# Optimization experiments

Measured on AMD Instinct MI355X. Metric: run time of the kernel, lower is better.

## Reference

```python
import jax, jax.numpy as jnp
from jax import lax
import numpy as np

B, T_IN, T_OUT = 16, 16, 16
C, H, W = 3, 64, 64
ZDIM, HID = 128, 512
DN = ('NCHW', 'OIHW', 'NCHW')


def setup_inputs() -> dict:
    key = jax.random.key(0)
    ks = iter(jax.random.split(key, 64))
    rn = lambda shape, s: jax.random.normal(next(ks), shape, jnp.float32) * s
    cs, ls = 0.05, 0.04  # conv / lstm weight scales
    inp = {
        'video': jax.random.uniform(next(ks), (B, T_IN, C, H, W), jnp.float32),
        'target_len': T_OUT,
        'ec1_w': rn((32, 3, 4, 4), cs),   'ec1_b': jnp.zeros((32,)),
        'ec2_w': rn((64, 32, 4, 4), cs),  'ec2_b': jnp.zeros((64,)),
        'ec3_w': rn((128, 64, 4, 4), cs), 'ec3_b': jnp.zeros((128,)),
        'ec4_w': rn((256, 128, 4, 4), cs),'ec4_b': jnp.zeros((256,)),
        'fcmu_w': rn((ZDIM, 4096), 0.02), 'fcmu_b': jnp.zeros((ZDIM,)),
        'dfc_w': rn((4096, ZDIM), 0.02),  'dfc_b': jnp.zeros((4096,)),
        'dt1_w': rn((128, 256, 4, 4), cs),'dt1_b': jnp.zeros((128,)),
        'dt2_w': rn((64, 128, 4, 4), cs), 'dt2_b': jnp.zeros((64,)),
        'dt3_w': rn((32, 64, 4, 4), cs),  'dt3_b': jnp.zeros((32,)),
        'dt4_w': rn((3, 32, 4, 4), cs),   'dt4_b': jnp.zeros((3,)),
        'wih_e': rn((4 * HID, ZDIM), ls), 'whh_e': rn((4 * HID, HID), ls),
        'bih_e': jnp.zeros((4 * HID,)),   'bhh_e': jnp.zeros((4 * HID,)),
        'wih_d': rn((4 * HID, ZDIM), ls), 'whh_d': rn((4 * HID, HID), ls),
        'bih_d': jnp.zeros((4 * HID,)),   'bhh_d': jnp.zeros((4 * HID,)),
        'fc_w': rn((ZDIM, HID), ls),      'fc_b': jnp.zeros((ZDIM,)),
    }
    return inp


def _conv(x, w, b):
    y = lax.conv_general_dilated(x, w, (2, 2), ((1, 1), (1, 1)), dimension_numbers=DN)
    return y + b[None, :, None, None]


def _convt(x, w, b):
    # transposed conv (stride 2, k=4, p=1) as input-dilated conv: out = 2*in
    y = lax.conv_general_dilated(x, w, (1, 1), ((2, 2), (2, 2)),
                                 lhs_dilation=(2, 2), dimension_numbers=DN)
    return y + b[None, :, None, None]


def _lstm_cell(x, h, c, wih, whh, bih, bhh):
    g = x @ wih.T + h @ whh.T + bih + bhh  # [N, 4H]
    i, f, gg, o = jnp.split(g, 4, axis=-1)  # torch gate order i,f,g,o
    c = jax.nn.sigmoid(f) * c + jax.nn.sigmoid(i) * jnp.tanh(gg)
    h = jax.nn.sigmoid(o) * jnp.tanh(c)
    return h, c


def reference(video, target_len,
              ec1_w, ec1_b, ec2_w, ec2_b, ec3_w, ec3_b, ec4_w, ec4_b,
              fcmu_w, fcmu_b, dfc_w, dfc_b,
              dt1_w, dt1_b, dt2_w, dt2_b, dt3_w, dt3_b, dt4_w, dt4_b,
              wih_e, whh_e, bih_e, bhh_e, wih_d, whh_d, bih_d, bhh_d,
              fc_w, fc_b):
    b, t = video.shape[:2]

    def encode(frames):  # [N, 3, 64, 64] -> [N, ZDIM] (z = mu, deterministic)
        x = jax.nn.relu(_conv(frames, ec1_w, ec1_b))
        x = jax.nn.relu(_conv(x, ec2_w, ec2_b))
        x = jax.nn.relu(_conv(x, ec3_w, ec3_b))
        x = jax.nn.relu(_conv(x, ec4_w, ec4_b))  # [N, 256, 4, 4]
        x = x.reshape(x.shape[0], -1)
        return x @ fcmu_w.T + fcmu_b

    def decode(z):  # [N, ZDIM] -> [N, 3, 64, 64]
        x = jax.nn.relu(z @ dfc_w.T + dfc_b).reshape(-1, 256, 4, 4)
        x = jax.nn.relu(_convt(x, dt1_w, dt1_b))
        x = jax.nn.relu(_convt(x, dt2_w, dt2_b))
        x = jax.nn.relu(_convt(x, dt3_w, dt3_b))
        return jax.nn.sigmoid(_convt(x, dt4_w, dt4_b))

    z = encode(video.reshape(b * t, C, H, W)).reshape(b, t, ZDIM)

    # encoder LSTM over input sequence
    def enc_step(carry, x_t):
        h, c = carry
        h, c = _lstm_cell(x_t, h, c, wih_e, whh_e, bih_e, bhh_e)
        return (h, c), None
    h0 = jnp.zeros((b, HID), video.dtype)
    (h, c), _ = lax.scan(enc_step, (h0, h0), z.transpose(1, 0, 2))

    def dec_step(carry, _):
        hh, cc, x = carry
        hh, cc = _lstm_cell(x, hh, cc, wih_d, whh_d, bih_d, bhh_d)
        out = hh @ fc_w.T + fc_b
        return (hh, cc, out), out
    _, zs = lax.scan(dec_step, (h, c, z[:, -1]), None, length=target_len)
    zs = zs.transpose(1, 0, 2).reshape(b * target_len, ZDIM)

    predicted = decode(zs).reshape(b, target_len, C, H, W)
    return predicted
```

## Files before the change

kernel.cpp:

```cpp
#include <hip/hip_runtime.h>
#include <math.h>


typedef float f32x4 __attribute__((ext_vector_type(4)));
typedef short bf16x8 __attribute__((ext_vector_type(8)));

__device__ __forceinline__ float sig_(float x) { return 1.f / (1.f + expf(-x)); }
__device__ __forceinline__ float dot4(float4 a, float4 b) {
    return a.x * b.x + a.y * b.y + a.z * b.z + a.w * b.w;
}
__device__ __forceinline__ int orig_row(int c) {
    return ((c >> 2) & 3) * 512 + (c >> 4) * 4 + (c & 3);
}
__device__ __forceinline__ unsigned short f2bf(float f) {
    unsigned int b = __float_as_uint(f);
    return (unsigned short)((b + 0x7fffu + ((b >> 16) & 1u)) >> 16);
}
__device__ __forceinline__ float bf2f(unsigned short h) {
    return __uint_as_float(((unsigned int)h) << 16);
}
__device__ __forceinline__ float4 bf4_to_f4(uint2 u) {
    float4 r;
    r.x = __uint_as_float((u.x & 0xffffu) << 16);
    r.y = __uint_as_float(u.x & 0xffff0000u);
    r.z = __uint_as_float((u.y & 0xffffu) << 16);
    r.w = __uint_as_float(u.y & 0xffff0000u);
    return r;
}

template<int CIP, int HI, int WI, int CO, int MREP, int WM, int WN, int MODE, int SRCF32>
__global__ __launch_bounds__(64 * WM * WN)
void conv_mfma(const unsigned short* __restrict__ Ahi, const float* __restrict__ Af,
               const unsigned short* __restrict__ WB, const float* __restrict__ bias,
               unsigned short* __restrict__ Yhi) {
    constexpr int K    = CIP * (MODE ? 4 : 16);
    constexpr int K32  = K / 32;
    constexpr int NI   = 2 * MREP;
    constexpr int TAPS = MODE ? 4 : 16;
    constexpr int CC   = (CIP >= 32) ? CIP / 32 : 1;
    constexpr int HO   = MODE ? HI * 2 : HI / 2;
    constexpr int WO   = MODE ? WI * 2 : WI / 2;
    constexpr int SH   = MODE ? HI : HI / 2;
    constexpr int SW   = MODE ? WI : WI / 2;
    constexpr int HWS  = SH * SW;
    constexpr int MT   = (256 * HWS) / (32 * MREP * WM);
    constexpr int NT   = CO / (32 * WN);
    constexpr int PLANE = CO * K;

    int bid = blockIdx.x;
    int mt = bid % MT; bid /= MT;
    int nt = bid % NT; int par = bid / NT;
    int p = par >> 1, q = par & 1;

    int tid = threadIdx.x;
    int lane = tid & 63, wid = tid >> 6;
    int wm = wid % WM, wn = wid / WM;
    int mbase = mt * (32 * MREP * WM) + wm * (32 * MREP);
    int nbase = nt * (32 * WN) + wn * 32;
    int lm = lane & 15, lg = lane >> 4;

    int ani[NI], asy[NI], asx[NI];
#pragma unroll
    for (int i = 0; i < NI; ++i) {
        int m = mbase + 16 * i + lm;
        ani[i] = m / HWS; int r = m % HWS; asy[i] = r / SW; asx[i] = r % SW;
    }

    f32x4 acc[NI][2];
#pragma unroll
    for (int i = 0; i < NI; ++i)
#pragma unroll
        for (int j = 0; j < 2; ++j)
#pragma unroll
            for (int e = 0; e < 4; ++e) acc[i][j][e] = 0.f;

    const unsigned short* WBp = WB + (long)par * 2 * PLANE;

    if constexpr (SRCF32) {
        for (int kb = 0; kb < K; kb += 32) {
            int k0 = kb + lg * 8;
            int t0 = k0 >> 2;
            bf16x8 ah[NI];
#pragma unroll
            for (int i = 0; i < NI; ++i) {
                float f[8];
#pragma unroll
                for (int h = 0; h < 2; ++h) {
                    int tap = t0 + h;
                    int ih = 2 * asy[i] + (tap >> 2) - 1;
                    int iw = 2 * asx[i] + (tap & 3) - 1;
                    float4 v = {0.f, 0.f, 0.f, 0.f};
                    if ((unsigned)ih < (unsigned)HI && (unsigned)iw < (unsigned)WI)
                        v = *(const float4*)(Af + (((long)ani[i] * HI + ih) * WI + iw) * 4);
                    f[h * 4 + 0] = v.x; f[h * 4 + 1] = v.y;
                    f[h * 4 + 2] = v.z; f[h * 4 + 3] = v.w;
                }
#pragma unroll
                for (int e = 0; e < 8; ++e) ah[i][e] = (short)f2bf(f[e]);
            }
            bf16x8 bh[2], bl[2];
#pragma unroll
            for (int j = 0; j < 2; ++j) {
                long bidx = ((long)((nbase >> 4) + j) * K32 + (kb >> 5)) * 512 + lane * 8;
                bh[j] = *(const bf16x8*)(WBp + bidx);
                bl[j] = *(const bf16x8*)(WBp + PLANE + bidx);
            }
#pragma unroll
            for (int i = 0; i < NI; ++i)
#pragma unroll
                for (int j = 0; j < 2; ++j) {
                    acc[i][j] = __builtin_amdgcn_mfma_f32_16x16x32_bf16(ah[i], bh[j], acc[i][j], 0, 0, 0);
                    acc[i][j] = __builtin_amdgcn_mfma_f32_16x16x32_bf16(ah[i], bl[j], acc[i][j], 0, 0, 0);
                }
        }
    } else {
        long abase[NI]; unsigned vmask[NI];
#pragma unroll
        for (int i = 0; i < NI; ++i) {
            abase[i] = (long)ani[i] * HI * WI * CIP;
            unsigned vm = 0;
#pragma unroll
            for (int t = 0; t < TAPS; ++t) {
                int iy, ix;
                if constexpr (MODE == 0) {
                    iy = 2 * asy[i] + (t >> 2) - 1; ix = 2 * asx[i] + (t & 3) - 1;
                } else {
                    iy = asy[i] + p + (t >> 1) - 1; ix = asx[i] + q + (t & 1) - 1;
                }
                if (iy >= 0 && iy < HI && ix >= 0 && ix < WI) vm |= (1u << t);
            }
            vmask[i] = vm;
        }
#pragma unroll 2
        for (int tap = 0; tap < TAPS; ++tap) {
            int dy, dx;
            if constexpr (MODE == 0) { dy = (tap >> 2) - 1; dx = (tap & 3) - 1; }
            else { dy = p + (tap >> 1) - 1; dx = q + (tap & 1) - 1; }
            long roff[NI]; unsigned msk[NI];
#pragma unroll
            for (int i = 0; i < NI; ++i) {
                int iy = (MODE == 0 ? 2 * asy[i] : asy[i]) + dy;
                int ix = (MODE == 0 ? 2 * asx[i] : asx[i]) + dx;
                int iyc = min(max(iy, 0), HI - 1);
                int ixc = min(max(ix, 0), WI - 1);
                roff[i] = abase[i] + ((long)iyc * WI + ixc) * CIP + lg * 8;
                msk[i] = ((vmask[i] >> tap) & 1u) ? 0xffffffffu : 0u;
            }
#pragma unroll
            for (int cc = 0; cc < CC; ++cc) {
                int kb32 = tap * CC + cc;
                bf16x8 ah[NI];
#pragma unroll
                for (int i = 0; i < NI; ++i) {
                    uint4 u = *(const uint4*)(Ahi + roff[i] + cc * 32);
                    u.x &= msk[i]; u.y &= msk[i]; u.z &= msk[i]; u.w &= msk[i];
                    ah[i] = *(bf16x8*)&u;
                }
                bf16x8 bh[2], bl[2];
#pragma unroll
                for (int j = 0; j < 2; ++j) {
                    long bidx = ((long)((nbase >> 4) + j) * K32 + kb32) * 512 + lane * 8;
                    bh[j] = *(const bf16x8*)(WBp + bidx);
                    bl[j] = *(const bf16x8*)(WBp + PLANE + bidx);
                }
#pragma unroll
                for (int i = 0; i < NI; ++i)
#pragma unroll
                    for (int j = 0; j < 2; ++j) {
                        acc[i][j] = __builtin_amdgcn_mfma_f32_16x16x32_bf16(ah[i], bh[j], acc[i][j], 0, 0, 0);
                        acc[i][j] = __builtin_amdgcn_mfma_f32_16x16x32_bf16(ah[i], bl[j], acc[i][j], 0, 0, 0);
                    }
            }
        }
    }

#pragma unroll
    for (int i = 0; i < NI; ++i)
#pragma unroll
        for (int j = 0; j < 2; ++j)
#pragma unroll
            for (int r = 0; r < 4; ++r) {
                int m = mbase + 16 * i + lg * 4 + r;
                int co = nbase + 16 * j + lm;
                float v = fmaxf(acc[i][j][r] + bias[co], 0.f);
                long off;
                if constexpr (MODE == 0) {
                    off = (long)m * CO + co;
                } else {
                    int ni = m / HWS; int rm = m % HWS;
                    int oy = 2 * (rm / SW) + p, ox = 2 * (rm % SW) + q;
                    off = (((long)ni * HO + oy) * WO + ox) * CO + co;
                }
                Yhi[off] = f2bf(v);
            }
}

__global__ __launch_bounds__(128)
void dt4_tiled(const unsigned short* __restrict__ Xh,
               const float4* __restrict__ Wd, const float* __restrict__ bias,
               float* __restrict__ out) {
    __shared__ uint2 xt[8 * 205];
    int bid = blockIdx.x;
    int n = bid >> 3, yg = bid & 7;
    int y0 = yg * 4;
    int tid = threadIdx.x;
    long nb = (long)n * 32768;
    for (int j = tid; j < 1632; j += 128) {
        int c4 = j & 7; int pos = j >> 3;
        int r = pos / 34, cc = pos % 34;
        int ih = y0 - 1 + r, iw = cc - 1;
        uint2 u = {0u, 0u};
        if ((unsigned)ih < 32u && (unsigned)iw < 32u)
            u = *(const uint2*)(Xh + nb + ((long)ih * 32 + iw) * 32 + c4 * 4);
        xt[c4 * 205 + pos] = u;
    }
    __syncthreads();
    int ly = tid >> 5, lx = tid & 31;
    float acc[3][4];
#pragma unroll
    for (int j = 0; j < 3; ++j) {
        float b = bias[j];
#pragma unroll
        for (int par = 0; par < 4; ++par) acc[j][par] = b;
    }
#pragma unroll
    for (int ci4 = 0; ci4 < 8; ++ci4) {
        float4 xv[9];
        int base = ci4 * 205 + ly * 34 + lx;
#pragma unroll
        for (int r = 0; r < 3; ++r)
#pragma unroll
            for (int c = 0; c < 3; ++c)
                xv[r * 3 + c] = bf4_to_f4(xt[base + r * 34 + c]);
        const float4* wp = Wd + ci4 * 48;
#pragma unroll
        for (int j = 0; j < 3; ++j)
#pragma unroll
            for (int par = 0; par < 4; ++par) {
                int p = par >> 1, q = par & 1;
#pragma unroll
                for (int t4 = 0; t4 < 4; ++t4) {
                    int dh = t4 >> 1, dw = t4 & 1;
                    acc[j][par] += dot4(xv[(p + dh) * 3 + (q + dw)],
                                        wp[(j * 4 + par) * 4 + t4]);
                }
            }
    }
    int yy = y0 + ly, xx = lx;
#pragma unroll
    for (int j = 0; j < 3; ++j)
#pragma unroll
        for (int p = 0; p < 2; ++p) {
            float2 v;
            v.x = sig_(acc[j][p * 2 + 0]);
            v.y = sig_(acc[j][p * 2 + 1]);
            *(float2*)(out + (((long)n * 3 + j) * 64 + 2 * yy + p) * 64 + 2 * xx) = v;
        }
}

__global__ void prep_packs(const float* __restrict__ ec3_w, const float* __restrict__ ec4_w,
                           const float* __restrict__ dt1_w, const float* __restrict__ dt2_w,
                           unsigned short* __restrict__ WBe3, unsigned short* __restrict__ WBe4,
                           unsigned short* __restrict__ WBd1, unsigned short* __restrict__ WBd2) {
    int idx = blockIdx.x * 256 + threadIdx.x;
    if (idx < 131072) {
        int li = idx;
        int j = li & 7, lane = (li >> 3) & 63;
        int kb = (li >> 9) & 31, nt = li >> 14;
        int k = kb * 32 + (lane >> 4) * 8 + j;
        int tap = k >> 6, ci = k & 63;
        int co = nt * 16 + (lane & 15);
        float f = ec3_w[((long)co * 64 + ci) * 16 + tap];
        unsigned short hi = f2bf(f);
        WBe3[li] = hi; WBe3[131072 + li] = f2bf(f - bf2f(hi));
    } else if (idx < 655360) {
        int li = idx - 131072;
        int j = li & 7, lane = (li >> 3) & 63;
        int kb = (li >> 9) & 63, nt = li >> 15;
        int k = kb * 32 + (lane >> 4) * 8 + j;
        int tap = k >> 7, ci = k & 127;
        int co = nt * 16 + (lane & 15);
        float f = ec4_w[((long)co * 128 + ci) * 16 + tap];
        unsigned short hi = f2bf(f);
        WBe4[li] = hi; WBe4[524288 + li] = f2bf(f - bf2f(hi));
    } else if (idx < 1179648) {
        int li = idx - 655360;
        int par = li >> 17; int rem = li & 131071;
        int j = rem & 7, lane = (rem >> 3) & 63;
        int kb = (rem >> 9) & 31, nt = rem >> 14;
        int k = kb * 32 + (lane >> 4) * 8 + j;
        int t4 = k >> 8, ci = k & 255;
        int p = par >> 1, q = par & 1, dh = t4 >> 1, dw = t4 & 1;
        int tap = (p + 2 * dh) * 4 + (q + 2 * dw);
        int co = nt * 16 + (lane & 15);
        float f = dt1_w[((long)co * 256 + ci) * 16 + tap];
        unsigned short hi = f2bf(f);
        WBd1[(long)par * 262144 + rem] = hi;
        WBd1[(long)par * 262144 + 131072 + rem] = f2bf(f - bf2f(hi));
    } else if (idx < 1310720) {
        int li = idx - 1179648;
        int par = li >> 15; int rem = li & 32767;
        int j = rem & 7, lane = (rem >> 3) & 63;
        int kb = (rem >> 9) & 15, nt = rem >> 13;
        int k = kb * 32 + (lane >> 4) * 8 + j;
        int t4 = k >> 7, ci = k & 127;
        int p = par >> 1, q = par & 1, dh = t4 >> 1, dw = t4 & 1;
        int tap = (p + 2 * dh) * 4 + (q + 2 * dw);
        int co = nt * 16 + (lane & 15);
        float f = dt2_w[((long)co * 128 + ci) * 16 + tap];
        unsigned short hi = f2bf(f);
        WBd2[(long)par * 65536 + rem] = hi;
        WBd2[(long)par * 65536 + 32768 + rem] = f2bf(f - bf2f(hi));
    }
}

__global__ void prep_tail(const float* __restrict__ ec1_w, const float* __restrict__ ec2_w,
                          const float* __restrict__ dt3_w, const float* __restrict__ dt4_w,
                          unsigned short* __restrict__ WBe1, unsigned short* __restrict__ WBe2,
                          unsigned short* __restrict__ WBd3, float4* __restrict__ WTd4) {
    int idx = blockIdx.x * 256 + threadIdx.x;
    if (idx < 2048) {
        int li = idx;
        int j = li & 7, lane = (li >> 3) & 63;
        int kb = (li >> 9) & 1, nt = li / 1024;
        int k = kb * 32 + (lane >> 4) * 8 + j;
        int tap = k >> 2, ci = k & 3;
        int co = nt * 16 + (lane & 15);
        float f = (ci < 3) ? ec1_w[((long)co * 3 + ci) * 16 + tap] : 0.f;
        unsigned short hi = f2bf(f);
        WBe1[li] = hi; WBe1[2048 + li] = f2bf(f - bf2f(hi));
    } else if (idx < 34816) {
        int li = idx - 2048;
        int j = li & 7, lane = (li >> 3) & 63;
        int kb = (li >> 9) & 15, nt = li / 8192;
        int k = kb * 32 + (lane >> 4) * 8 + j;
        int tap = k >> 5, ci = k & 31;
        int co = nt * 16 + (lane & 15);
        float f = ec2_w[((long)co * 32 + ci) * 16 + tap];
        unsigned short hi = f2bf(f);
        WBe2[li] = hi; WBe2[32768 + li] = f2bf(f - bf2f(hi));
    } else if (idx < 67584) {
        int li = idx - 34816;
        int par = li >> 13; int rem = li & 8191;
        int j = rem & 7, lane = (rem >> 3) & 63;
        int kb = (rem >> 9) & 7, nt = rem >> 12;
        int k = kb * 32 + (lane >> 4) * 8 + j;
        int t4 = k >> 6, ci = k & 63;
        int p = par >> 1, q = par & 1, dh = t4 >> 1, dw = t4 & 1;
        int tap = (p + 2 * dh) * 4 + (q + 2 * dw);
        int co = nt * 16 + (lane & 15);
        float f = dt3_w[((long)co * 64 + ci) * 16 + tap];
        unsigned short hi = f2bf(f);
        WBd3[par * 16384 + rem] = hi;
        WBd3[par * 16384 + 8192 + rem] = f2bf(f - bf2f(hi));
    } else if (idx < 67968) {
        int li = idx - 67584;
        int t4 = li & 3, par = (li >> 2) & 3;
        int co = (li >> 4) % 3, ci4 = (li >> 4) / 3;
        int p = par >> 1, q = par & 1, dh = t4 >> 1, dw = t4 & 1;
        int tap = (p + 2 * dh) * 4 + (q + 2 * dw);
        float4 v; float* pv = (float*)&v;
#pragma unroll
        for (int l = 0; l < 4; ++l)
            pv[l] = dt4_w[((long)co * 32 + ci4 * 4 + l) * 16 + tap];
        WTd4[li] = v;
    }
}

__global__ void prep_r1(const float* __restrict__ wih_e, const float* __restrict__ wih_d,
                        const float* __restrict__ fc_w,
                        const float* __restrict__ bih_d, const float* __restrict__ bhh_d,
                        const float* __restrict__ fc_b,
                        const float* __restrict__ fcmu_w, const float* __restrict__ dfc_w,
                        const float* __restrict__ dfc_b,
                        float* __restrict__ WIHP_E, float* __restrict__ WIHP_D,
                        float* __restrict__ FCP, float* __restrict__ BIASDC,
                        float* __restrict__ FCMUP, float* __restrict__ DFCP,
                        float* __restrict__ DFCB) {
    int idx = blockIdx.x * 256 + threadIdx.x;
    if (idx < 262144) {
        int c = idx & 2047, m = idx >> 11;
        WIHP_E[idx] = wih_e[orig_row(c) * 128 + m];
    } else if (idx < 524288) {
        int li = idx - 262144;
        int c = li & 2047, m = li >> 11;
        WIHP_D[li] = wih_d[orig_row(c) * 128 + m];
    } else if (idx < 589824) {
        int li = idx - 524288;
        int r = li & 127, c = li >> 7;
        FCP[li] = fc_w[(long)r * 512 + c];
    } else if (idx < 591872) {
        int c = idx - 589824;
        int orow = orig_row(c);
        float s = bih_d[orow] + bhh_d[orow];
        for (int m = 0; m < 128; ++m) s += fc_b[m] * wih_d[orow * 128 + m];
        BIASDC[c] = s;
    } else if (idx < 1116160) {
        int li = idx - 591872;
        int j = li & 127, k = li >> 7;
        FCMUP[li] = fcmu_w[(long)j * 4096 + (k & 255) * 16 + (k >> 8)];
    } else {
        int li = idx - 1116160;
        int j = li & 4095, m = li >> 12;
        int jc = (j & 255) * 16 + (j >> 8);
        DFCP[li] = dfc_w[(long)jc * 128 + m];
        if (li < 4096) DFCB[li] = dfc_b[(li & 255) * 16 + (li >> 8)];
    }
}

__global__ void to_nhwc4v(const float* __restrict__ v, float4* __restrict__ out) {
    int idx = blockIdx.x * 256 + threadIdx.x;
    int w = idx & 63, h = (idx >> 6) & 63, n = idx >> 12;
    long base = (long)n * 12288 + h * 64 + w;
    float4 o;
    o.x = v[base];
    o.y = v[base + 4096];
    o.z = v[base + 8192];
    o.w = 0.f;
    out[idx] = o;
}

__global__ void pack_whh(const float* __restrict__ whh, float4* __restrict__ out) {
    int idx = blockIdx.x * 256 + threadIdx.x;
    int c = idx & 2047, k4 = idx >> 11;
    const float4* src = (const float4*)(whh + orig_row(c) * 512);
    out[idx] = src[k4];
}

__global__ __launch_bounds__(256)
void merge_dc(const float* __restrict__ wih_d, const float* __restrict__ fc_w,
              const float* __restrict__ whh_d, float* __restrict__ out) {
    int cb = (blockIdx.x >> 3) * 64, kb = (blockIdx.x & 7) * 64;
    int tid = threadIdx.x;
    int cgl = (tid & 15) * 4, kgl = (tid >> 4) * 4;
    __shared__ float At[64][65];
    __shared__ float Bt[64][65];
    float acc[4][4] = {};
    for (int mc = 0; mc < 128; mc += 64) {
        __syncthreads();
        for (int i = tid; i < 4096; i += 256) {
            int cl = i >> 6, m = i & 63;
            At[cl][m] = wih_d[orig_row(cb + cl) * 128 + mc + m];
            Bt[cl][m] = fc_w[(mc + cl) * 512 + kb + m];
        }
        __syncthreads();
        for (int m = 0; m < 64; ++m) {
            float a[4], b[4];
#pragma unroll
            for (int i = 0; i < 4; ++i) { a[i] = At[cgl + i][m]; b[i] = Bt[m][kgl + i]; }
#pragma unroll
            for (int i = 0; i < 4; ++i)
#pragma unroll
                for (int j = 0; j < 4; ++j) acc[i][j] += a[i] * b[j];
        }
    }
    for (int i = 0; i < 4; ++i) {
        int c = cb + cgl + i; int orow = orig_row(c);
        for (int j = 0; j < 4; ++j) {
            int k = kb + kgl + j;
            out[((k >> 2) * 2048 + c) * 4 + (k & 3)] = acc[i][j] + whh_d[orow * 512 + k];
        }
    }
}

__global__ __launch_bounds__(512)
void gx2_kernel(const float* __restrict__ Z,
                const float* __restrict__ wE, const float* __restrict__ biE,
                const float* __restrict__ bhE,
                const float* __restrict__ wD, const float* __restrict__ biD,
                const float* __restrict__ bhD,
                float* __restrict__ gxe, float* __restrict__ gxd0) {
    __shared__ float zl[2048];
    int bid = blockIdx.x, tid = threadIdx.x;
    if (bid < 128) {
        int rg = bid >> 2, cch = bid & 3;
        for (int i = tid; i < 1024; i += 512)
            zl[i] = Z[(long)(rg * 8 + (i >> 7)) * 128 + (i & 127)];
        __syncthreads();
        int c = cch * 512 + tid;
        int orow = orig_row(c);
        float bsum = biE[orow] + bhE[orow];
        float acc[8];
#pragma unroll
        for (int r = 0; r < 8; ++r) acc[r] = bsum;
        for (int m = 0; m < 128; ++m) {
            float wv = wE[m * 2048 + c];
#pragma unroll
            for (int r = 0; r < 8; ++r) acc[r] += zl[r * 128 + m] * wv;
        }
        for (int r = 0; r < 8; ++r) gxe[(long)(rg * 8 + r) * 2048 + c] = acc[r];
    } else {
        int cch = bid - 128;
        for (int i = tid; i < 2048; i += 512)
            zl[i] = Z[(long)((i >> 7) * 16 + 15) * 128 + (i & 127)];
        __syncthreads();
        int c = cch * 512 + tid;
        int orow = orig_row(c);
        float bsum = biD[orow] + bhD[orow];
        float acc[16];
#pragma unroll
        for (int r = 0; r < 16; ++r) acc[r] = bsum;
        for (int m = 0; m < 128; ++m) {
            float wv = wD[m * 2048 + c];
#pragma unroll
            for (int r = 0; r < 16; ++r) acc[r] += zl[r * 128 + m] * wv;
        }
        for (int r = 0; r < 16; ++r) gxd0[(long)r * 2048 + c] = acc[r];
    }
}

__global__ __launch_bounds__(256)
void lstm_step(const float4* __restrict__ wh4, const float* __restrict__ gadd,
               int gstride, const float* __restrict__ h_in, float* __restrict__ h_out,
               float* __restrict__ cst, float* __restrict__ hall) {
    __shared__ float hs[8192];
    __shared__ float gb[16][16];
    int tid = threadIdx.x;
    float4* hs4 = (float4*)hs;
    const float4* hi4 = (const float4*)h_in;
#pragma unroll
    for (int i = 0; i < 8; ++i) hs4[tid + 256 * i] = hi4[tid + 256 * i];
    __syncthreads();
    int col = tid & 15, n = tid >> 4;
    int cg = blockIdx.x * 16 + col;
    float acc = gadd[n * gstride + cg];
    const float4* wp = wh4 + cg;
    const float4* hv = (const float4*)(hs + n * 512);
#pragma unroll 8
    for (int k4 = 0; k4 < 128; ++k4) {
        float4 wv = wp[(long)k4 * 2048];
        float4 h4 = hv[k4];
        acc += wv.x * h4.x + wv.y * h4.y + wv.z * h4.z + wv.w * h4.w;
    }
    gb[n][col] = acc;
    __syncthreads();
    if (col < 4) {
        int j = blockIdx.x * 4 + col;
        float gi = sig_(gb[n][col]);
        float gf = sig_(gb[n][col + 4]);
        float gg = tanhf(gb[n][col + 8]);
        float go = sig_(gb[n][col + 12]);
        int idx = n * 512 + j;
        float cv = gf * cst[idx] + gi * gg;
        cst[idx] = cv;
        float hvv = go * tanhf(cv);
        h_out[idx] = hvv;
        if (hall) hall[idx] = hvv;
    }
}

__global__ __launch_bounds__(512)
void fcmu_part(const unsigned short* __restrict__ xh,
               const float* __restrict__ wP, float* __restrict__ part) {
    int rg = blockIdx.x >> 4, ks = blockIdx.x & 15;
    int tid = threadIdx.x;
    __shared__ float xls[16 * 256];
    for (int i = tid; i < 4096; i += 512) {
        long gi = (long)(rg * 16 + (i >> 8)) * 4096 + ks * 256 + (i & 255);
        xls[i] = bf2f(xh[gi]);
    }
    __syncthreads();
    int j = tid & 127, rq = tid >> 7;
    float acc[4] = {0, 0, 0, 0};
    for (int k = 0; k < 256; ++k) {
        float wv = wP[(ks * 256 + k) * 128 + j];
#pragma unroll
        for (int i = 0; i < 4; ++i) acc[i] += xls[(rq + 4 * i) * 256 + k] * wv;
    }
    for (int i = 0; i < 4; ++i)
        part[((long)ks * 256 + rg * 16 + rq + 4 * i) * 128 + j] = acc[i];
}

__global__ void fcmu_red(const float* __restrict__ part, const float* __restrict__ b,
                         float* __restrict__ z) {
    int idx = blockIdx.x * 256 + threadIdx.x;
    float s = b[idx & 127];
    for (int k = 0; k < 16; ++k) s += part[k * 32768 + idx];
    z[idx] = s;
}

__global__ __launch_bounds__(512)
void zs_k(const float* __restrict__ hall, const float* __restrict__ fcP,
          const float* __restrict__ fcb, float* __restrict__ zs) {
    int t = blockIdx.x >> 2, nq = blockIdx.x & 3;
    int tid = threadIdx.x;
    __shared__ float hs[4 * 512];
    const float* h = hall + (long)t * 8192 + nq * 2048;
    for (int i = tid; i < 2048; i += 512) hs[i] = h[i];
    __syncthreads();
    int j = tid & 127, nl = tid >> 7;
    float a0 = 0.f, a1 = 0.f, a2 = 0.f, a3 = 0.f;
    const float* hr = hs + nl * 512;
    for (int k = 0; k < 512; k += 4) {
        a0 += hr[k] * fcP[k * 128 + j];
        a1 += hr[k + 1] * fcP[(k + 1) * 128 + j];
        a2 += hr[k + 2] * fcP[(k + 2) * 128 + j];
        a3 += hr[k + 3] * fcP[(k + 3) * 128 + j];
    }
    int n = nq * 4 + nl;
    zs[((long)n * 16 + t) * 128 + j] = (a0 + a1) + (a2 + a3) + fcb[j];
}

__global__ __launch_bounds__(256)
void dfc_k(const float* __restrict__ zs, const float* __restrict__ dP,
           const float* __restrict__ db, unsigned short* __restrict__ outh) {
    int rg = blockIdx.x >> 4, jc = blockIdx.x & 15;
    int tid = threadIdx.x;
    __shared__ float zl[512];
    for (int i = tid; i < 512; i += 256) zl[i] = zs[(long)rg * 512 + i];
    __syncthreads();
    int j = jc * 256 + tid;
    float acc[4] = {0.f, 0.f, 0.f, 0.f};
    for (int m = 0; m < 128; ++m) {
        float wv = dP[(long)m * 4096 + j];
#pragma unroll
        for (int r = 0; r < 4; ++r) acc[r] += zl[r * 128 + m] * wv;
    }
    float bv = db[j];
    for (int r = 0; r < 4; ++r) {
        float v = fmaxf(acc[r] + bv, 0.f);
        outh[(long)(rg * 4 + r) * 4096 + j] = f2bf(v);
    }
}

extern "C" void kernel_launch(void* const* d_in, const int* in_sizes, int n_in,
                              void* d_out, int out_size, void* d_ws, size_t ws_size,
                              hipStream_t stream) {
    (void)in_sizes; (void)n_in; (void)out_size; (void)ws_size;
    const float* video  = (const float*)d_in[0];
    const float* ec1_w  = (const float*)d_in[2];  const float* ec1_b = (const float*)d_in[3];
    const float* ec2_w  = (const float*)d_in[4];  const float* ec2_b = (const float*)d_in[5];
    const float* ec3_w  = (const float*)d_in[6];  const float* ec3_b = (const float*)d_in[7];
    const float* ec4_w  = (const float*)d_in[8];  const float* ec4_b = (const float*)d_in[9];
    const float* fcmu_w = (const float*)d_in[10]; const float* fcmu_b = (const float*)d_in[11];
    const float* dfc_w  = (const float*)d_in[12]; const float* dfc_b = (const float*)d_in[13];
    const float* dt1_w  = (const float*)d_in[14]; const float* dt1_b = (const float*)d_in[15];
    const float* dt2_w  = (const float*)d_in[16]; const float* dt2_b = (const float*)d_in[17];
    const float* dt3_w  = (const float*)d_in[18]; const float* dt3_b = (const float*)d_in[19];
    const float* dt4_w  = (const float*)d_in[20]; const float* dt4_b = (const float*)d_in[21];
    const float* wih_e  = (const float*)d_in[22]; const float* whh_e = (const float*)d_in[23];
    const float* bih_e  = (const float*)d_in[24]; const float* bhh_e = (const float*)d_in[25];
    const float* wih_d  = (const float*)d_in[26]; const float* whh_d = (const float*)d_in[27];
    const float* bih_d  = (const float*)d_in[28]; const float* bhh_d = (const float*)d_in[29];
    const float* fc_w   = (const float*)d_in[30]; const float* fc_b  = (const float*)d_in[31];

    char* wsb = (char*)d_ws;
    unsigned short* B1h = (unsigned short*)wsb;
    float*          X0f = (float*)(wsb + 33554432);
    unsigned short* B2h = (unsigned short*)(wsb + 33554432);
    unsigned short* B3h = (unsigned short*)(wsb + 50331648);
    unsigned short* B4h = (unsigned short*)(wsb + 58720256);
    float* R1f    = (float*)wsb;
    float* WH4_E  = R1f;
    float* WH4_DC = R1f + 1048576;
    float* WIHP_E = R1f + 2097152;
    float* WIHP_D = R1f + 2359296;
    float* GX_E   = R1f + 2621440;
    float* GX_D0  = R1f + 3145728;
    float* BIASDC = R1f + 3178496;
    float* HA     = R1f + 3180544;
    float* HB     = R1f + 3188736;
    float* CB     = R1f + 3196928;
    float* HALL   = R1f + 3205120;
    float* FCMUP  = R1f + 3336192;
    float* FCP    = R1f + 4122624;
    float* DFCP   = R1f + 4188160;
    float* DFCB   = R1f + 4712448;
    float* Z      = R1f + 4716544;
    float* ZS     = R1f + 4749312;
    unsigned short* WBe3 = (unsigned short*)(R1f + 4782080);
    unsigned short* WBe4 = (unsigned short*)(R1f + 4913152);
    unsigned short* WBd1 = (unsigned short*)(R1f + 5437440);
    unsigned short* WBd2 = (unsigned short*)(R1f + 5961728);
    float* ZPART  = R1f + 6092800;
    unsigned short* WBe1 = (unsigned short*)(wsb + 62914560);
    unsigned short* WBe2 = (unsigned short*)(wsb + 62922752);
    unsigned short* WBd3 = (unsigned short*)(wsb + 63053824);
    float*          WTd4 = (float*)(wsb + 63184896);

    prep_tail<<<266, 256, 0, stream>>>(ec1_w, ec2_w, dt3_w, dt4_w,
                                       WBe1, WBe2, WBd3, (float4*)WTd4);
    to_nhwc4v<<<4096, 256, 0, stream>>>(video, (float4*)X0f);
    conv_mfma<4, 64, 64, 32, 2, 4, 1, 0, 1><<<1024, 256, 0, stream>>>(
        nullptr, X0f, WBe1, ec1_b, B1h);
    conv_mfma<32, 32, 32, 64, 1, 2, 2, 0, 0><<<1024, 256, 0, stream>>>(
        B1h, nullptr, WBe2, ec2_b, B2h);

    prep_r1<<<6408, 256, 0, stream>>>(wih_e, wih_d, fc_w, bih_d, bhh_d, fc_b,
                                      fcmu_w, dfc_w, dfc_b,
                                      WIHP_E, WIHP_D, FCP, BIASDC, FCMUP, DFCP, DFCB);
    prep_packs<<<5120, 256, 0, stream>>>(ec3_w, ec4_w, dt1_w, dt2_w,
                                         WBe3, WBe4, WBd1, WBd2);
    pack_whh<<<1024, 256, 0, stream>>>(whh_e, (float4*)WH4_E);
    merge_dc<<<256, 256, 0, stream>>>(wih_d, fc_w, whh_d, WH4_DC);
    hipMemsetAsync(HA, 0, 3 * 8192 * sizeof(float), stream);

    conv_mfma<64, 16, 16, 128, 1, 2, 2, 0, 0><<<512, 256, 0, stream>>>(
        B2h, nullptr, WBe3, ec3_b, B3h);
    conv_mfma<128, 8, 8, 256, 1, 1, 2, 0, 0><<<512, 128, 0, stream>>>(
        B3h, nullptr, WBe4, ec4_b, B4h);
    fcmu_part<<<256, 512, 0, stream>>>(B4h, FCMUP, ZPART);
    fcmu_red<<<128, 256, 0, stream>>>(ZPART, fcmu_b, Z);

    gx2_kernel<<<132, 512, 0, stream>>>(Z, WIHP_E, bih_e, bhh_e,
                                        WIHP_D, bih_d, bhh_d, GX_E, GX_D0);

    float* hin = HA; float* hout = HB;
    for (int t = 0; t < 16; ++t) {
        lstm_step<<<128, 256, 0, stream>>>((const float4*)WH4_E, GX_E + t * 2048, 32768,
                                           hin, hout, CB, (float*)nullptr);
        float* tmp = hin; hin = hout; hout = tmp;
    }
    pack_whh<<<1024, 256, 0, stream>>>(whh_d, (float4*)WH4_E);
    lstm_step<<<128, 256, 0, stream>>>((const float4*)WH4_E, GX_D0, 2048,
                                       hin, hout, CB, HALL);
    { float* tmp = hin; hin = hout; hout = tmp; }
    for (int t = 1; t < 16; ++t) {
        lstm_step<<<128, 256, 0, stream>>>((const float4*)WH4_DC, BIASDC, 0,
                                           hin, hout, CB, HALL + t * 8192);
        float* tmp = hin; hin = hout; hout = tmp;
    }
    zs_k<<<64, 512, 0, stream>>>(HALL, FCP, fc_b, ZS);

    dfc_k<<<1024, 256, 0, stream>>>(ZS, DFCP, DFCB, B4h);
    conv_mfma<256, 4, 4, 128, 1, 2, 2, 1, 0><<<512, 256, 0, stream>>>(
        B4h, nullptr, WBd1, dt1_b, B3h);
    conv_mfma<128, 8, 8, 64, 1, 2, 2, 1, 0><<<1024, 256, 0, stream>>>(
        B3h, nullptr, WBd2, dt2_b, B2h);
    conv_mfma<64, 16, 16, 32, 2, 4, 1, 1, 0><<<1024, 256, 0, stream>>>(
        B2h, nullptr, WBd3, dt3_b, B1h);
    dt4_tiled<<<2048, 128, 0, stream>>>(B1h, (const float4*)WTd4, dt4_b, (float*)d_out);
}
```

Measured before the change: 601.5 us.

## Split LSTM step across twice the blocks with K-split and regrouped gate columns

After: 535.8 us. 10.9% less time.

```diff
diff --git a/kernel.cpp b/kernel.cpp
--- a/kernel.cpp
+++ b/kernel.cpp
@@ -10,7 +10,7 @@
     return a.x * b.x + a.y * b.y + a.z * b.z + a.w * b.w;
 }
 __device__ __forceinline__ int orig_row(int c) {
-    return ((c >> 2) & 3) * 512 + (c >> 4) * 4 + (c & 3);
+    return ((c >> 1) & 3) * 512 + (c >> 3) * 2 + (c & 1);
 }
 __device__ __forceinline__ unsigned short f2bf(float f) {
     unsigned int b = __float_as_uint(f);
@@ -514,33 +514,41 @@
                int gstride, const float* __restrict__ h_in, float* __restrict__ h_out,
                float* __restrict__ cst, float* __restrict__ hall) {
     __shared__ float hs[8192];
-    __shared__ float gb[16][16];
+    __shared__ float gp[2][16][8];
     int tid = threadIdx.x;
     float4* hs4 = (float4*)hs;
     const float4* hi4 = (const float4*)h_in;
 #pragma unroll
     for (int i = 0; i < 8; ++i) hs4[tid + 256 * i] = hi4[tid + 256 * i];
     __syncthreads();
-    int col = tid & 15, n = tid >> 4;
-    int cg = blockIdx.x * 16 + col;
-    float acc = gadd[n * gstride + cg];
+    int col = tid & 7, n = (tid >> 3) & 15, kh = tid >> 7;
+    int cg = blockIdx.x * 8 + col;
     const float4* wp = wh4 + cg;
     const float4* hv = (const float4*)(hs + n * 512);
+    float acc = 0.f;
+    int k0 = kh * 64;
 #pragma unroll 8
-    for (int k4 = 0; k4 < 128; ++k4) {
+    for (int k4 = k0; k4 < k0 + 64; ++k4) {
         float4 wv = wp[(long)k4 * 2048];
         float4 h4 = hv[k4];
         acc += wv.x * h4.x + wv.y * h4.y + wv.z * h4.z + wv.w * h4.w;
     }
-    gb[n][col] = acc;
+    gp[kh][n][col] = acc;
     __syncthreads();
-    if (col < 4) {
-        int j = blockIdx.x * 4 + col;
-        float gi = sig_(gb[n][col]);
-        float gf = sig_(gb[n][col + 4]);
-        float gg = tanhf(gb[n][col + 8]);
-        float go = sig_(gb[n][col + 12]);
-        int idx = n * 512 + j;
+    if (tid < 128) {
+        int cc = tid & 7, nn = tid >> 3;
+        gp[0][nn][cc] = gp[0][nn][cc] + gp[1][nn][cc]
+                      + gadd[nn * gstride + blockIdx.x * 8 + cc];
+    }
+    __syncthreads();
+    if (tid < 32) {
+        int c2 = tid & 1, n2 = tid >> 1;
+        float gi = sig_(gp[0][n2][c2]);
+        float gf = sig_(gp[0][n2][c2 + 2]);
+        float gg = tanhf(gp[0][n2][c2 + 4]);
+        float go = sig_(gp[0][n2][c2 + 6]);
+        int j = blockIdx.x * 2 + c2;
+        int idx = n2 * 512 + j;
         float cv = gf * cst[idx] + gi * gg;
         cst[idx] = cv;
         float hvv = go * tanhf(cv);
@@ -673,6 +681,7 @@
     unsigned short* WBd1 = (unsigned short*)(R1f + 5437440);
     unsigned short* WBd2 = (unsigned short*)(R1f + 5961728);
     float* ZPART  = R1f + 6092800;
+    float* WH4_D0 = R1f + 6617088;
     unsigned short* WBe1 = (unsigned short*)(wsb + 62914560);
     unsigned short* WBe2 = (unsigned short*)(wsb + 62922752);
     unsigned short* WBd3 = (unsigned short*)(wsb + 63053824);
@@ -692,6 +701,7 @@
     prep_packs<<<5120, 256, 0, stream>>>(ec3_w, ec4_w, dt1_w, dt2_w,
                                          WBe3, WBe4, WBd1, WBd2);
     pack_whh<<<1024, 256, 0, stream>>>(whh_e, (float4*)WH4_E);
+    pack_whh<<<1024, 256, 0, stream>>>(whh_d, (float4*)WH4_D0);
     merge_dc<<<256, 256, 0, stream>>>(wih_d, fc_w, whh_d, WH4_DC);
     hipMemsetAsync(HA, 0, 3 * 8192 * sizeof(float), stream);
 
@@ -707,16 +717,15 @@
 
     float* hin = HA; float* hout = HB;
     for (int t = 0; t < 16; ++t) {
-        lstm_step<<<128, 256, 0, stream>>>((const float4*)WH4_E, GX_E + t * 2048, 32768,
+        lstm_step<<<256, 256, 0, stream>>>((const float4*)WH4_E, GX_E + t * 2048, 32768,
                                            hin, hout, CB, (float*)nullptr);
         float* tmp = hin; hin = hout; hout = tmp;
     }
-    pack_whh<<<1024, 256, 0, stream>>>(whh_d, (float4*)WH4_E);
-    lstm_step<<<128, 256, 0, stream>>>((const float4*)WH4_E, GX_D0, 2048,
+    lstm_step<<<256, 256, 0, stream>>>((const float4*)WH4_D0, GX_D0, 2048,
                                        hin, hout, CB, HALL);
     { float* tmp = hin; hin = hout; hout = tmp; }
     for (int t = 1; t < 16; ++t) {
-        lstm_step<<<128, 256, 0, stream>>>((const float4*)WH4_DC, BIASDC, 0,
+        lstm_step<<<256, 256, 0, stream>>>((const float4*)WH4_DC, BIASDC, 0,
                                            hin, hout, CB, HALL + t * 8192);
         float* tmp = hin; hin = hout; hout = tmp;
     }
```
